# Kernel optimization log

Hardware: AMD Instinct MI355X
Metric: run time of the kernel (lower is better)

## Reference

```python
import jax, jax.numpy as jnp
import numpy as np

T, B, I, H = 512, 128, 256, 256  # seq_len, batch, input_size, hidden_size


def setup_inputs() -> dict:
    key = jax.random.key(0)
    ks = jax.random.split(key, 7)
    s = 1.0 / np.sqrt(H)  # PyTorch LSTM init scale
    return {
        "x": jax.random.normal(ks[0], (T, B, I), dtype=jnp.float32),
        "h0": jax.random.normal(ks[1], (1, B, H), dtype=jnp.float32),
        "c0": jax.random.normal(ks[2], (1, B, H), dtype=jnp.float32),
        "W_ih": jax.random.uniform(ks[3], (4 * H, I), jnp.float32, -s, s),
        "W_hh": jax.random.uniform(ks[4], (4 * H, H), jnp.float32, -s, s),
        "b_ih": jax.random.uniform(ks[5], (4 * H,), jnp.float32, -s, s),
        "b_hh": jax.random.uniform(ks[6], (4 * H,), jnp.float32, -s, s),
    }


def reference(x, h0, c0, W_ih, W_hh, b_ih, b_hh):
    # Precompute input contribution for all timesteps in one big GEMM: [T,B,4H]
    gates_x = jnp.einsum("tbi,gi->tbg", x, W_ih) + b_ih + b_hh

    def step(carry, gx):
        h, c = carry
        g = gx + h @ W_hh.T  # [B,4H]
        i, f, gg, o = jnp.split(g, 4, axis=-1)  # PyTorch gate order i,f,g,o
        i = jax.nn.sigmoid(i)
        f = jax.nn.sigmoid(f)
        gg = jnp.tanh(gg)
        o = jax.nn.sigmoid(o)
        c_new = f * c + i * gg
        h_new = o * jnp.tanh(c_new)
        return (h_new, c_new), h_new

    (h_T, c_T), ys = jax.lax.scan(step, (h0[0], c0[0]), gates_x)
    return ys, h_T[None], c_T[None]
```

## Files before the change

kernel.cpp:

```cpp
#include <hip/hip_runtime.h>
#include <hip/hip_bf16.h>
#include <math.h>

#define T_STEPS 512
#define BATCH   128
#define ISZ     256
#define HSZ     256
#define G4      1024
#define WIN     16
#define XPAD    4
#define KR      16

__global__ __launch_bounds__(256) void prep_tables(
    const float* __restrict__ W_hh, const float* __restrict__ W_ih,
    float* __restrict__ WT4h, float* __restrict__ WT4i) {
  int idx = blockIdx.x * 256 + threadIdx.x;
  int k4 = idx >> 12;
  int r  = (idx >> 2) & 1023;
  int c  = idx & 3;
  WT4h[idx] = W_hh[r * 256 + k4 * 4 + c];
  WT4i[idx] = W_ih[r * 256 + k4 * 4 + c];
}

__global__ __launch_bounds__(512, 2) void lstm_fused(
    const float* __restrict__ x,
    const float* __restrict__ WT4h,
    const float* __restrict__ WT4i,
    const float* __restrict__ bih, const float* __restrict__ bhh,
    const float* __restrict__ h0, const float* __restrict__ c0,
    float* __restrict__ out) {
  __shared__ __align__(16) float x_lds[WIN][HSZ + XPAD];
  __shared__ __align__(16) float gx_lds[WIN][G4];
  __shared__ __align__(16) float h_lds[HSZ];
  __shared__ __align__(16) float g_lds[G4];

  const int b = blockIdx.x;
  const int t = threadIdx.x;
  const int r = t;
  const int rg = t >> 2;
  const int sg = t & 3;

  float bias_g[8];
  #pragma unroll
  for (int i = 0; i < 8; ++i) {
    int rr = rg * 8 + i;
    bias_g[i] = bih[rr] + bhh[rr];
  }

  float4 wr0[KR], wr1[KR];
  #pragma unroll
  for (int k = 0; k < KR; ++k) {
    wr0[k] = *reinterpret_cast<const float4*>(&WT4h[(size_t)k * 4096 + r * 4]);
    wr1[k] = *reinterpret_cast<const float4*>(&WT4h[(size_t)k * 4096 + (r + 512) * 4]);
  }

  if (t < HSZ) h_lds[t] = h0[b * HSZ + t];
  float c = (t < HSZ) ? c0[b * HSZ + t] : 0.f;
  __syncthreads();

  for (int w = 0; w < T_STEPS / WIN; ++w) {
    const int s0 = w * WIN;

    #pragma unroll
    for (int j = 0; j < 2; ++j) {
      int f = t + j * 512;
      int s = f >> 6, kq = f & 63;
      float4 v = reinterpret_cast<const float4*>(x)[((size_t)(s0 + s) * BATCH + b) * 64 + kq];
      *reinterpret_cast<float4*>(&x_lds[s][kq * 4]) = v;
    }
    __syncthreads();

    float acc[8][4];
    #pragma unroll
    for (int i = 0; i < 8; ++i)
      #pragma unroll
      for (int ss = 0; ss < 4; ++ss) acc[i][ss] = bias_g[i];

    #pragma unroll 4
    for (int k4 = 0; k4 < 64; ++k4) {
      float4 xv[4];
      #pragma unroll
      for (int ss = 0; ss < 4; ++ss)
        xv[ss] = *reinterpret_cast<const float4*>(&x_lds[sg * 4 + ss][k4 * 4]);
      #pragma unroll
      for (int i = 0; i < 8; ++i) {
        float4 wv = *reinterpret_cast<const float4*>(&WT4i[(size_t)k4 * 4096 + (rg * 8 + i) * 4]);
        #pragma unroll
        for (int ss = 0; ss < 4; ++ss)
          acc[i][ss] += wv.x * xv[ss].x + wv.y * xv[ss].y + wv.z * xv[ss].z + wv.w * xv[ss].w;
      }
    }
    #pragma unroll
    for (int i = 0; i < 8; ++i)
      #pragma unroll
      for (int ss = 0; ss < 4; ++ss)
        gx_lds[sg * 4 + ss][rg * 8 + i] = acc[i][ss];
    __syncthreads();

    for (int s = 0; s < WIN; ++s) {
      float a0 = gx_lds[s][r];
      float a1 = gx_lds[s][r + 512];

      float sa0 = 0.f, sa1 = 0.f;
      #pragma unroll 8
      for (int k4 = KR; k4 < 64; ++k4) {
        float4 w0 = *reinterpret_cast<const float4*>(&WT4h[(size_t)k4 * 4096 + r * 4]);
        float4 w1 = *reinterpret_cast<const float4*>(&WT4h[(size_t)k4 * 4096 + (r + 512) * 4]);
        float4 hv = *reinterpret_cast<const float4*>(&h_lds[k4 * 4]);
        sa0 += w0.x * hv.x + w0.y * hv.y + w0.z * hv.z + w0.w * hv.w;
        sa1 += w1.x * hv.x + w1.y * hv.y + w1.z * hv.z + w1.w * hv.w;
      }
      #pragma unroll
      for (int k = 0; k < KR; ++k) {
        float4 hv = *reinterpret_cast<const float4*>(&h_lds[k * 4]);
        a0 += wr0[k].x * hv.x + wr0[k].y * hv.y + wr0[k].z * hv.z + wr0[k].w * hv.w;
        a1 += wr1[k].x * hv.x + wr1[k].y * hv.y + wr1[k].z * hv.z + wr1[k].w * hv.w;
      }
      a0 += sa0;
      a1 += sa1;
      g_lds[r] = a0;
      g_lds[r + 512] = a1;
      __syncthreads();

      if (t < HSZ) {
        float gi = g_lds[t];
        float gf = g_lds[t + 256];
        float gg = g_lds[t + 512];
        float go = g_lds[t + 768];
        gi = 1.f / (1.f + expf(-gi));
        gf = 1.f / (1.f + expf(-gf));
        go = 1.f / (1.f + expf(-go));
        gg = tanhf(gg);
        c = gf * c + gi * gg;
        float h = go * tanhf(c);
        h_lds[t] = h;
        out[(size_t)(s0 + s) * BATCH * HSZ + b * HSZ + t] = h;
      }
      __syncthreads();
    }
  }

  if (t < HSZ) {
    out[(size_t)T_STEPS * BATCH * HSZ + b * HSZ + t] = h_lds[t];
    out[(size_t)T_STEPS * BATCH * HSZ + (size_t)BATCH * HSZ + b * HSZ + t] = c;
  }
}

extern "C" void kernel_launch(void* const* d_in, const int* in_sizes, int n_in,
                              void* d_out, int out_size, void* d_ws, size_t ws_size,
                              hipStream_t stream) {
  const float* x   = (const float*)d_in[0];
  const float* h0  = (const float*)d_in[1];
  const float* c0  = (const float*)d_in[2];
  const float* Wih = (const float*)d_in[3];
  const float* Whh = (const float*)d_in[4];
  const float* bih = (const float*)d_in[5];
  const float* bhh = (const float*)d_in[6];
  float* out = (float*)d_out;

  char* ws = (char*)d_ws;
  float* WT4h = (float*)ws;
  float* WT4i = (float*)(ws + (1 << 20));

  prep_tables<<<1024, 256, 0, stream>>>(Whh, Wih, WT4h, WT4i);
  lstm_fused<<<BATCH, 512, 0, stream>>>(x, WT4h, WT4i, bih, bhh, h0, c0, out);
}
```

Measured before the change: 5.676 ms.

## Split recurrent K dimension across four workgroups with flag-synchronized partial sums

Adds a new LSTM kernel that launches 256 workgroups: each handles two batch rows and a quarter of the hidden-state K slice. Each workgroup writes its partial gate sums to global memory, publishes a per-step flag, spins until its three peers have published, and then sums all four partials. The aim is to spread the serial recurrent matvec across four times as many CUs and have each workgroup cover two batch rows so weight loads are reused. In exchange it adds a global-memory round-trip and an inter-workgroup spin barrier on every timestep, and it relies on all 256 workgroups being co-resident. The previous single-workgroup-per-batch kernel stays as a fallback when the workspace is too small.

```diff
diff --git a/kernel.cpp b/kernel.cpp
--- a/kernel.cpp
+++ b/kernel.cpp
@@ -7,9 +7,8 @@
 #define ISZ     256
 #define HSZ     256
 #define G4      1024
-#define WIN     16
-#define XPAD    4
-#define KR      16
+#define KSL     16
+#define QWIN    8
 
 __global__ __launch_bounds__(256) void prep_tables(
     const float* __restrict__ W_hh, const float* __restrict__ W_ih,
@@ -22,45 +21,193 @@
   WT4i[idx] = W_ih[r * 256 + k4 * 4 + c];
 }
 
-__global__ __launch_bounds__(512, 2) void lstm_fused(
+__global__ __launch_bounds__(512, 2) void lstm_quad(
     const float* __restrict__ x,
     const float* __restrict__ WT4h,
     const float* __restrict__ WT4i,
     const float* __restrict__ bih, const float* __restrict__ bhh,
     const float* __restrict__ h0, const float* __restrict__ c0,
-    float* __restrict__ out) {
+    float* __restrict__ out,
+    unsigned int* __restrict__ flags,
+    float* __restrict__ part) {
+  __shared__ __align__(16) float x_lds[2][QWIN][68];
+  __shared__ __align__(16) float gx_lds[2][QWIN][G4];
+  __shared__ __align__(16) float h_lds[2][HSZ];
+  __shared__ __align__(16) float g_lds[2][G4];
+
+  const int wg = blockIdx.x;
+  const int m  = wg >> 6;
+  const int q  = wg & 63;
+  const int b0 = q * 2;
+  const int t  = threadIdx.x;
+  const int r  = t;
+  const int rg = t >> 2;
+  const int sg = t & 3;
+  const int k4lo = m * KSL;
+  const int klo  = k4lo * 4;
+  const int ur = t >> 8;
+  const int uc = t & 255;
+
+  float bias_g[8];
+  #pragma unroll
+  for (int i = 0; i < 8; ++i)
+    bias_g[i] = (m == 0) ? (bih[rg * 8 + i] + bhh[rg * 8 + i]) : 0.f;
+
+  h_lds[ur][uc] = h0[(b0 + ur) * HSZ + uc];
+  float c = c0[(b0 + ur) * HSZ + uc];
+  __syncthreads();
+
+  for (int w = 0; w < T_STEPS / QWIN; ++w) {
+    const int s0 = w * QWIN;
+
+    if (t < 256) {
+      int brow = t >> 7, s = (t >> 4) & 7, f4 = t & 15;
+      float4 v = *reinterpret_cast<const float4*>(
+          &x[((size_t)(s0 + s) * BATCH + b0 + brow) * ISZ + klo + f4 * 4]);
+      *reinterpret_cast<float4*>(&x_lds[brow][s][f4 * 4]) = v;
+    }
+    __syncthreads();
+
+    float acc[8][2][2];
+    #pragma unroll
+    for (int i = 0; i < 8; ++i)
+      #pragma unroll
+      for (int s2 = 0; s2 < 2; ++s2)
+        #pragma unroll
+        for (int br = 0; br < 2; ++br) acc[i][s2][br] = bias_g[i];
+
+    #pragma unroll 4
+    for (int k4 = 0; k4 < KSL; ++k4) {
+      float4 xv[2][2];
+      #pragma unroll
+      for (int s2 = 0; s2 < 2; ++s2)
+        #pragma unroll
+        for (int br = 0; br < 2; ++br)
+          xv[s2][br] = *reinterpret_cast<const float4*>(&x_lds[br][sg * 2 + s2][k4 * 4]);
+      #pragma unroll
+      for (int i = 0; i < 8; ++i) {
+        float4 wv = *reinterpret_cast<const float4*>(
+            &WT4i[(size_t)(k4lo + k4) * 4096 + (rg * 8 + i) * 4]);
+        #pragma unroll
+        for (int s2 = 0; s2 < 2; ++s2)
+          #pragma unroll
+          for (int br = 0; br < 2; ++br)
+            acc[i][s2][br] += wv.x * xv[s2][br].x + wv.y * xv[s2][br].y +
+                              wv.z * xv[s2][br].z + wv.w * xv[s2][br].w;
+      }
+    }
+    #pragma unroll
+    for (int i = 0; i < 8; ++i)
+      #pragma unroll
+      for (int s2 = 0; s2 < 2; ++s2)
+        #pragma unroll
+        for (int br = 0; br < 2; ++br)
+          gx_lds[br][sg * 2 + s2][rg * 8 + i] = acc[i][s2][br];
+    __syncthreads();
+
+    for (int s = 0; s < QWIN; ++s) {
+      const int step = s0 + s;
+      const int par  = step & 1;
+
+      float a00 = gx_lds[0][s][r], a01 = gx_lds[0][s][r + 512];
+      float a10 = gx_lds[1][s][r], a11 = gx_lds[1][s][r + 512];
+
+      #pragma unroll 8
+      for (int k4 = k4lo; k4 < k4lo + KSL; ++k4) {
+        float4 w0 = *reinterpret_cast<const float4*>(&WT4h[(size_t)k4 * 4096 + r * 4]);
+        float4 w1 = *reinterpret_cast<const float4*>(&WT4h[(size_t)k4 * 4096 + (r + 512) * 4]);
+        float4 ha = *reinterpret_cast<const float4*>(&h_lds[0][k4 * 4]);
+        float4 hb = *reinterpret_cast<const float4*>(&h_lds[1][k4 * 4]);
+        a00 += w0.x * ha.x + w0.y * ha.y + w0.z * ha.z + w0.w * ha.w;
+        a01 += w1.x * ha.x + w1.y * ha.y + w1.z * ha.z + w1.w * ha.w;
+        a10 += w0.x * hb.x + w0.y * hb.y + w0.z * hb.z + w0.w * hb.w;
+        a11 += w1.x * hb.x + w1.y * hb.y + w1.z * hb.z + w1.w * hb.w;
+      }
+
+      float* pb = part + ((size_t)(q * 4 + m) * 2 + par) * 2048;
+      __hip_atomic_store(&pb[r],          a00, __ATOMIC_RELAXED, __HIP_MEMORY_SCOPE_AGENT);
+      __hip_atomic_store(&pb[r + 512],    a01, __ATOMIC_RELAXED, __HIP_MEMORY_SCOPE_AGENT);
+      __hip_atomic_store(&pb[1024 + r],   a10, __ATOMIC_RELAXED, __HIP_MEMORY_SCOPE_AGENT);
+      __hip_atomic_store(&pb[1024 + r + 512], a11, __ATOMIC_RELAXED, __HIP_MEMORY_SCOPE_AGENT);
+      __syncthreads();
+      if (t == 0) {
+        __threadfence();
+        __hip_atomic_store(&flags[((q * 4 + m) * 2 + par) * 16], (unsigned)(step + 1),
+                           __ATOMIC_RELEASE, __HIP_MEMORY_SCOPE_AGENT);
+      }
+      if (t < 4) {
+        unsigned int* f = &flags[((q * 4 + t) * 2 + par) * 16];
+        int guard = 0;
+        while (__hip_atomic_load(f, __ATOMIC_ACQUIRE, __HIP_MEMORY_SCOPE_AGENT) <
+               (unsigned)(step + 1)) {
+          __builtin_amdgcn_s_sleep(1);
+          if (++guard > (1 << 26)) break;
+        }
+      }
+      __syncthreads();
+
+      float g00 = 0.f, g01 = 0.f, g10 = 0.f, g11 = 0.f;
+      #pragma unroll
+      for (int mm = 0; mm < 4; ++mm) {
+        float* pm = part + ((size_t)(q * 4 + mm) * 2 + par) * 2048;
+        g00 += __hip_atomic_load(&pm[r],            __ATOMIC_RELAXED, __HIP_MEMORY_SCOPE_AGENT);
+        g01 += __hip_atomic_load(&pm[r + 512],      __ATOMIC_RELAXED, __HIP_MEMORY_SCOPE_AGENT);
+        g10 += __hip_atomic_load(&pm[1024 + r],     __ATOMIC_RELAXED, __HIP_MEMORY_SCOPE_AGENT);
+        g11 += __hip_atomic_load(&pm[1024 + r + 512], __ATOMIC_RELAXED, __HIP_MEMORY_SCOPE_AGENT);
+      }
+      g_lds[0][r] = g00; g_lds[0][r + 512] = g01;
+      g_lds[1][r] = g10; g_lds[1][r + 512] = g11;
+      __syncthreads();
+
+      {
+        float gi = g_lds[ur][uc];
+        float gf = g_lds[ur][uc + 256];
+        float gg = g_lds[ur][uc + 512];
+        float go = g_lds[ur][uc + 768];
+        gi = 1.f / (1.f + expf(-gi));
+        gf = 1.f / (1.f + expf(-gf));
+        go = 1.f / (1.f + expf(-go));
+        gg = tanhf(gg);
+        c = gf * c + gi * gg;
+        float h = go * tanhf(c);
+        h_lds[ur][uc] = h;
+        if (m == 0)
+          out[(size_t)step * BATCH * HSZ + (b0 + ur) * HSZ + uc] = h;
+      }
+      __syncthreads();
+    }
+  }
+
+  if (m == 0) {
+    out[(size_t)T_STEPS * BATCH * HSZ + (b0 + ur) * HSZ + uc] = h_lds[ur][uc];
+    out[(size_t)T_STEPS * BATCH * HSZ + (size_t)BATCH * HSZ + (b0 + ur) * HSZ + uc] = c;
+  }
+}
+
+#define WIN  16
+#define XPAD 4
+__global__ __launch_bounds__(512, 2) void lstm_fused(
+    const float* __restrict__ x, const float* __restrict__ WT4h,
+    const float* __restrict__ WT4i, const float* __restrict__ bih,
+    const float* __restrict__ bhh, const float* __restrict__ h0,
+    const float* __restrict__ c0, float* __restrict__ out) {
   __shared__ __align__(16) float x_lds[WIN][HSZ + XPAD];
   __shared__ __align__(16) float gx_lds[WIN][G4];
   __shared__ __align__(16) float h_lds[HSZ];
   __shared__ __align__(16) float g_lds[G4];
-
   const int b = blockIdx.x;
   const int t = threadIdx.x;
   const int r = t;
   const int rg = t >> 2;
   const int sg = t & 3;
-
   float bias_g[8];
   #pragma unroll
-  for (int i = 0; i < 8; ++i) {
-    int rr = rg * 8 + i;
-    bias_g[i] = bih[rr] + bhh[rr];
-  }
-
-  float4 wr0[KR], wr1[KR];
-  #pragma unroll
-  for (int k = 0; k < KR; ++k) {
-    wr0[k] = *reinterpret_cast<const float4*>(&WT4h[(size_t)k * 4096 + r * 4]);
-    wr1[k] = *reinterpret_cast<const float4*>(&WT4h[(size_t)k * 4096 + (r + 512) * 4]);
-  }
-
+  for (int i = 0; i < 8; ++i) bias_g[i] = bih[rg * 8 + i] + bhh[rg * 8 + i];
   if (t < HSZ) h_lds[t] = h0[b * HSZ + t];
   float c = (t < HSZ) ? c0[b * HSZ + t] : 0.f;
   __syncthreads();
-
   for (int w = 0; w < T_STEPS / WIN; ++w) {
     const int s0 = w * WIN;
-
     #pragma unroll
     for (int j = 0; j < 2; ++j) {
       int f = t + j * 512;
@@ -69,13 +216,11 @@
       *reinterpret_cast<float4*>(&x_lds[s][kq * 4]) = v;
     }
     __syncthreads();
-
     float acc[8][4];
     #pragma unroll
     for (int i = 0; i < 8; ++i)
       #pragma unroll
       for (int ss = 0; ss < 4; ++ss) acc[i][ss] = bias_g[i];
-
     #pragma unroll 4
     for (int k4 = 0; k4 < 64; ++k4) {
       float4 xv[4];
@@ -96,37 +241,24 @@
       for (int ss = 0; ss < 4; ++ss)
         gx_lds[sg * 4 + ss][rg * 8 + i] = acc[i][ss];
     __syncthreads();
-
     for (int s = 0; s < WIN; ++s) {
       float a0 = gx_lds[s][r];
       float a1 = gx_lds[s][r + 512];
-
       float sa0 = 0.f, sa1 = 0.f;
       #pragma unroll 8
-      for (int k4 = KR; k4 < 64; ++k4) {
+      for (int k4 = 0; k4 < 64; ++k4) {
         float4 w0 = *reinterpret_cast<const float4*>(&WT4h[(size_t)k4 * 4096 + r * 4]);
         float4 w1 = *reinterpret_cast<const float4*>(&WT4h[(size_t)k4 * 4096 + (r + 512) * 4]);
         float4 hv = *reinterpret_cast<const float4*>(&h_lds[k4 * 4]);
         sa0 += w0.x * hv.x + w0.y * hv.y + w0.z * hv.z + w0.w * hv.w;
         sa1 += w1.x * hv.x + w1.y * hv.y + w1.z * hv.z + w1.w * hv.w;
       }
-      #pragma unroll
-      for (int k = 0; k < KR; ++k) {
-        float4 hv = *reinterpret_cast<const float4*>(&h_lds[k * 4]);
-        a0 += wr0[k].x * hv.x + wr0[k].y * hv.y + wr0[k].z * hv.z + wr0[k].w * hv.w;
-        a1 += wr1[k].x * hv.x + wr1[k].y * hv.y + wr1[k].z * hv.z + wr1[k].w * hv.w;
-      }
-      a0 += sa0;
-      a1 += sa1;
+      a0 += sa0; a1 += sa1;
       g_lds[r] = a0;
       g_lds[r + 512] = a1;
       __syncthreads();
-
       if (t < HSZ) {
-        float gi = g_lds[t];
-        float gf = g_lds[t + 256];
-        float gg = g_lds[t + 512];
-        float go = g_lds[t + 768];
+        float gi = g_lds[t], gf = g_lds[t + 256], gg = g_lds[t + 512], go = g_lds[t + 768];
         gi = 1.f / (1.f + expf(-gi));
         gf = 1.f / (1.f + expf(-gf));
         go = 1.f / (1.f + expf(-go));
@@ -139,7 +271,6 @@
       __syncthreads();
     }
   }
-
   if (t < HSZ) {
     out[(size_t)T_STEPS * BATCH * HSZ + b * HSZ + t] = h_lds[t];
     out[(size_t)T_STEPS * BATCH * HSZ + (size_t)BATCH * HSZ + b * HSZ + t] = c;
@@ -161,7 +292,17 @@
   char* ws = (char*)d_ws;
   float* WT4h = (float*)ws;
   float* WT4i = (float*)(ws + (1 << 20));
-
+  unsigned int* flags = (unsigned int*)(ws + (2 << 20));
+  float* part = (float*)(ws + (2 << 20) + (64 << 10));
+
+  const size_t NEED_QUAD = (size_t)(2 << 20) + (64 << 10) + (4 << 20);
   prep_tables<<<1024, 256, 0, stream>>>(Whh, Wih, WT4h, WT4i);
-  lstm_fused<<<BATCH, 512, 0, stream>>>(x, WT4h, WT4i, bih, bhh, h0, c0, out);
+
+  if (ws_size >= NEED_QUAD) {
+    hipMemsetAsync(flags, 0, 64 * 4 * 2 * 16 * sizeof(unsigned int), stream);
+    lstm_quad<<<256, 512, 0, stream>>>(x, WT4h, WT4i, bih, bhh, h0, c0, out,
+                                       flags, part);
+  } else {
+    lstm_fused<<<BATCH, 512, 0, stream>>>(x, WT4h, WT4i, bih, bhh, h0, c0, out);
+  }
 }
```

Result: slower. 8.230 ms (+45.0%).
